# Optimization experiments

Measured on AMD Instinct MI355X. Metric: run time of the kernel, lower is better.

## Reference

```python
import jax, jax.numpy as jnp
import numpy as np

NUM_CLASSES = 19

def setup_inputs() -> dict:
    key = jax.random.key(0)
    k1, k2 = jax.random.split(key)
    feats = jax.random.normal(k1, (8, 256, 128, 256), dtype=jnp.float32)
    y_down = jax.random.randint(k2, (8, 128, 256), 0, NUM_CLASSES, dtype=jnp.int64)
    return {"feats": feats, "y_down": y_down}

def reference(feats, y_down):
    # feats: [B, C, H, W]; y_down: [B, H, W] int labels in [0, NUM_CLASSES)
    B, C, H, W = feats.shape
    x = jnp.transpose(feats, (0, 2, 3, 1)).reshape(-1, C)   # [N, C], N = B*H*W
    seg = y_down.reshape(-1).astype(jnp.int32)              # [N]
    # per-class sum of feature vectors and pixel counts (fused segment reduce)
    sums = jax.ops.segment_sum(x, seg, num_segments=NUM_CLASSES)          # [K, C]
    counts = jax.ops.segment_sum(jnp.ones((x.shape[0],), x.dtype), seg,
                                 num_segments=NUM_CLASSES)                # [K]
    denom = jnp.maximum(counts, 1.0)
    nonempty = counts > 0
    # b_c: per-class mean feature vector (zeros for empty classes, which torch
    # returns as empty tensors)
    means = jnp.where(nonempty[:, None], sums / denom[:, None], 0.0)      # [K, C]
    # n_c: per-class mean of per-pixel L2 norms (detached in original)
    norms = jnp.linalg.norm(x, axis=1)                                    # [N]
    norm_sums = jax.ops.segment_sum(norms, seg, num_segments=NUM_CLASSES)
    norm_means = jnp.where(nonempty, norm_sums / denom, 0.0)              # [K]
    return means, norm_means
```

## Files before the change

### kernel.cpp

```cpp
#include <hip/hip_runtime.h>

#define NCLS 19
#define NCH  256
#define HW   (128 * 256)
#define NPIX (8 * HW)
#define P    32
#define NT   (NPIX / P)
#define TPAD 36
#define SPAD 33
#define SUMS (NCLS * NCH)
#define PN_NORM SUMS
#define PN_CNT  (SUMS + NCLS)
#define PSTRIDE 4928
#define GRID  512
#define TILES (NT / GRID)

__device__ __forceinline__ void bar_lds() {
    asm volatile("s_waitcnt lgkmcnt(0)" ::: "memory");
    __builtin_amdgcn_sched_barrier(0);
    __builtin_amdgcn_s_barrier();
    __builtin_amdgcn_sched_barrier(0);
}

__global__ __launch_bounds__(256) void accum_kernel(
    const float* __restrict__ feats, const int* __restrict__ labels,
    float* __restrict__ partials)
{
    __shared__ float tile[NCH * TPAD];
    __shared__ float accA[SUMS];
    __shared__ float accB[SUMS];
    __shared__ float sqpart[32 * SPAD];
    __shared__ float accN[NCLS];
    __shared__ float accC[NCLS];
    __shared__ int   lab_s[P];

    const int t = threadIdx.x;
    for (int j = t; j < SUMS; j += 256) { accA[j] = 0.f; accB[j] = 0.f; }
    if (t < NCLS) { accN[t] = 0.f; accC[t] = 0.f; }

    const int j4 = (t & 7) * 4, cb = t >> 3;
    float4 v4[8];
    int labv = 0;

    {
        const int p0 = blockIdx.x * P, b = p0 >> 15, hw0 = p0 & (HW - 1);
        const float* fb = feats + (size_t)b * NCH * HW + hw0;
        #pragma unroll
        for (int i = 0; i < 8; ++i)
            v4[i] = *reinterpret_cast<const float4*>(fb + (size_t)(i * 32 + cb) * HW + j4);
        if (t < P) labv = labels[p0 + t];
    }
    {
        float s0 = 0.f, s1 = 0.f, s2 = 0.f, s3 = 0.f;
        #pragma unroll
        for (int i = 0; i < 8; ++i) {
            const int c = i * 32 + cb;
            tile[c * TPAD + j4    ] = v4[i].x; tile[c * TPAD + j4 + 1] = v4[i].y;
            tile[c * TPAD + j4 + 2] = v4[i].z; tile[c * TPAD + j4 + 3] = v4[i].w;
            s0 += v4[i].x * v4[i].x; s1 += v4[i].y * v4[i].y;
            s2 += v4[i].z * v4[i].z; s3 += v4[i].w * v4[i].w;
        }
        sqpart[cb * SPAD + j4    ] = s0; sqpart[cb * SPAD + j4 + 1] = s1;
        sqpart[cb * SPAD + j4 + 2] = s2; sqpart[cb * SPAD + j4 + 3] = s3;
        if (t < P) lab_s[t] = labv;
    }
    __syncthreads();

    for (int it = 0; it < TILES; ++it) {
        if (it + 1 < TILES) {
            const int p0 = (blockIdx.x + (it + 1) * GRID) * P;
            const int b = p0 >> 15, hw0 = p0 & (HW - 1);
            const float* fb = feats + (size_t)b * NCH * HW + hw0;
            #pragma unroll
            for (int i = 0; i < 8; ++i)
                v4[i] = *reinterpret_cast<const float4*>(fb + (size_t)(i * 32 + cb) * HW + j4);
            if (t < P) labv = labels[p0 + t];
        }
        {
            float v[P];
            #pragma unroll
            for (int p = 0; p < P; ++p) v[p] = tile[t * TPAD + p];
            #pragma unroll
            for (int p = 0; p < P; p += 2) {
                const int k0 = lab_s[p], k1 = lab_s[p + 1];
                accA[k0 * NCH + t] += v[p];
                accB[k1 * NCH + t] += v[p + 1];
            }
        }
        if (t < P) {
            float s = 0.f;
            #pragma unroll
            for (int m = 0; m < 32; ++m) s += sqpart[m * SPAD + t];
            const int k = lab_s[t];
            unsafeAtomicAdd(&accN[k], sqrtf(s));
            unsafeAtomicAdd(&accC[k], 1.f);
        }
        bar_lds();
        if (it + 1 < TILES) {
            float s0 = 0.f, s1 = 0.f, s2 = 0.f, s3 = 0.f;
            #pragma unroll
            for (int i = 0; i < 8; ++i) {
                const int c = i * 32 + cb;
                tile[c * TPAD + j4    ] = v4[i].x; tile[c * TPAD + j4 + 1] = v4[i].y;
                tile[c * TPAD + j4 + 2] = v4[i].z; tile[c * TPAD + j4 + 3] = v4[i].w;
                s0 += v4[i].x * v4[i].x; s1 += v4[i].y * v4[i].y;
                s2 += v4[i].z * v4[i].z; s3 += v4[i].w * v4[i].w;
            }
            sqpart[cb * SPAD + j4    ] = s0; sqpart[cb * SPAD + j4 + 1] = s1;
            sqpart[cb * SPAD + j4 + 2] = s2; sqpart[cb * SPAD + j4 + 3] = s3;
            if (t < P) lab_s[t] = labv;
        }
        bar_lds();
    }

    float* op = partials + (size_t)blockIdx.x * PSTRIDE;
    for (int j = t; j < SUMS; j += 256) op[j] = accA[j] + accB[j];
    if (t < NCLS) { op[PN_NORM + t] = accN[t]; op[PN_CNT + t] = accC[t]; }
}

__global__ __launch_bounds__(256) void reduce_kernel(
    const float* __restrict__ partials, float* __restrict__ out)
{
    __shared__ float cred[NCLS][9];
    __shared__ float red[16][17];
    __shared__ float cnt_s[NCLS];
    const int t = threadIdx.x;

    if (t < NCLS * 8) {
        const int k = t >> 3, gl = t & 7;
        float c = 0.f;
        #pragma unroll 8
        for (int j = 0; j < 64; ++j)
            c += partials[(size_t)(gl + 8 * j) * PSTRIDE + PN_CNT + k];
        cred[k][gl] = c;
    }
    {
        const int ol = t & 15, gl = t >> 4;
        const int o = blockIdx.x * 16 + ol;
        float s = 0.f;
        if (o < PN_CNT) {
            #pragma unroll 8
            for (int j = 0; j < 32; ++j)
                s += partials[(size_t)(gl + 16 * j) * PSTRIDE + o];
        }
        red[gl][ol] = s;
    }
    __syncthreads();
    if (t < NCLS) {
        float c = 0.f;
        #pragma unroll
        for (int g = 0; g < 8; ++g) c += cred[t][g];
        cnt_s[t] = c;
    }
    __syncthreads();
    if (t < 16) {
        const int oo = blockIdx.x * 16 + t;
        if (oo < PN_CNT) {
            float tot = 0.f;
            #pragma unroll
            for (int g = 0; g < 16; ++g) tot += red[g][t];
            const int k = (oo < SUMS) ? (oo >> 8) : (oo - SUMS);
            const float c = cnt_s[k];
            out[oo] = (c > 0.f) ? tot / fmaxf(c, 1.f) : 0.f;
        }
    }
}

extern "C" void kernel_launch(void* const* d_in, const int* in_sizes, int n_in,
                              void* d_out, int out_size, void* d_ws, size_t ws_size,
                              hipStream_t stream) {
    const float* feats  = (const float*)d_in[0];
    const int*   labels = (const int*)d_in[1];
    float* out      = (float*)d_out;
    float* partials = (float*)d_ws;

    accum_kernel<<<GRID, 256, 0, stream>>>(feats, labels, partials);
    reduce_kernel<<<(PN_CNT + 15) / 16, 256, 0, stream>>>(partials, out);
}
```

Measured before the change: 66.45 us.

## Accumulate per-class feature sums with one-hot bf16 MFMA instead of LDS scatter

Per-class sums are now computed as a matrix product of a one-hot label matrix and the feature tile, using 32x32x16 bf16 MFMA with fp32 accumulation held in registers. The feature tile is stored in LDS as bf16 rather than fp32, and the two LDS accumulator arrays are removed. This is meant to remove the serialized LDS read-modify-write scatter adds and to halve LDS traffic for the tile. In exchange, the feature values entering the sums are rounded to bf16, which reduces accuracy of the means.

```diff
diff --git a/kernel.cpp b/kernel.cpp
--- a/kernel.cpp
+++ b/kernel.cpp
@@ -6,7 +6,7 @@
 #define NPIX (8 * HW)
 #define P    32
 #define NT   (NPIX / P)
-#define TPAD 36
+#define THP  36
 #define SPAD 33
 #define SUMS (NCLS * NCH)
 #define PN_NORM SUMS
@@ -15,6 +15,11 @@
 #define GRID  512
 #define TILES (NT / GRID)
 
+typedef __bf16 bf16x4v __attribute__((ext_vector_type(4)));
+typedef __bf16 bf16x8v __attribute__((ext_vector_type(8)));
+typedef float  f32x16v __attribute__((ext_vector_type(16)));
+typedef int    int4v   __attribute__((ext_vector_type(4)));
+
 __device__ __forceinline__ void bar_lds() {
     asm volatile("s_waitcnt lgkmcnt(0)" ::: "memory");
     __builtin_amdgcn_sched_barrier(0);
@@ -26,19 +31,22 @@
     const float* __restrict__ feats, const int* __restrict__ labels,
     float* __restrict__ partials)
 {
-    __shared__ float tile[NCH * TPAD];
-    __shared__ float accA[SUMS];
-    __shared__ float accB[SUMS];
-    __shared__ float sqpart[32 * SPAD];
-    __shared__ float accN[NCLS];
-    __shared__ float accC[NCLS];
-    __shared__ int   lab_s[P];
+    __shared__ __bf16 tileh[NCH * THP];
+    __shared__ float  sqpart[32 * SPAD];
+    __shared__ float  accN[NCLS];
+    __shared__ float  accC[NCLS];
+    __shared__ int    lab_s[P];
 
     const int t = threadIdx.x;
-    for (int j = t; j < SUMS; j += 256) { accA[j] = 0.f; accB[j] = 0.f; }
     if (t < NCLS) { accN[t] = 0.f; accC[t] = 0.f; }
 
     const int j4 = (t & 7) * 4, cb = t >> 3;
+    const int w = t >> 6, l = t & 63, h = l >> 5, col = l & 31;
+    const int c0 = w * 64 + col;
+    const int c1 = c0 + 32;
+    const __bf16 ONE = (__bf16)1.0f, ZER = (__bf16)0.0f;
+
+    f32x16v d0 = {}, d1 = {};
     float4 v4[8];
     int labv = 0;
 
@@ -55,8 +63,8 @@
         #pragma unroll
         for (int i = 0; i < 8; ++i) {
             const int c = i * 32 + cb;
-            tile[c * TPAD + j4    ] = v4[i].x; tile[c * TPAD + j4 + 1] = v4[i].y;
-            tile[c * TPAD + j4 + 2] = v4[i].z; tile[c * TPAD + j4 + 3] = v4[i].w;
+            bf16x4v hv = { (__bf16)v4[i].x, (__bf16)v4[i].y, (__bf16)v4[i].z, (__bf16)v4[i].w };
+            *reinterpret_cast<bf16x4v*>(&tileh[c * THP + j4]) = hv;
             s0 += v4[i].x * v4[i].x; s1 += v4[i].y * v4[i].y;
             s2 += v4[i].z * v4[i].z; s3 += v4[i].w * v4[i].w;
         }
@@ -76,16 +84,24 @@
                 v4[i] = *reinterpret_cast<const float4*>(fb + (size_t)(i * 32 + cb) * HW + j4);
             if (t < P) labv = labels[p0 + t];
         }
-        {
-            float v[P];
-            #pragma unroll
-            for (int p = 0; p < P; ++p) v[p] = tile[t * TPAD + p];
-            #pragma unroll
-            for (int p = 0; p < P; p += 2) {
-                const int k0 = lab_s[p], k1 = lab_s[p + 1];
-                accA[k0 * NCH + t] += v[p];
-                accB[k1 * NCH + t] += v[p + 1];
-            }
+        #pragma unroll
+        for (int s = 0; s < 2; ++s) {
+            const int pb = s * 16 + h * 8;
+            const int4v lq0 = *reinterpret_cast<const int4v*>(&lab_s[pb]);
+            const int4v lq1 = *reinterpret_cast<const int4v*>(&lab_s[pb + 4]);
+            bf16x8v af;
+            af[0] = (lq0[0] == col) ? ONE : ZER;  af[1] = (lq0[1] == col) ? ONE : ZER;
+            af[2] = (lq0[2] == col) ? ONE : ZER;  af[3] = (lq0[3] == col) ? ONE : ZER;
+            af[4] = (lq1[0] == col) ? ONE : ZER;  af[5] = (lq1[1] == col) ? ONE : ZER;
+            af[6] = (lq1[2] == col) ? ONE : ZER;  af[7] = (lq1[3] == col) ? ONE : ZER;
+            const bf16x4v b0l = *reinterpret_cast<const bf16x4v*>(&tileh[c0 * THP + pb]);
+            const bf16x4v b0h = *reinterpret_cast<const bf16x4v*>(&tileh[c0 * THP + pb + 4]);
+            const bf16x4v b1l = *reinterpret_cast<const bf16x4v*>(&tileh[c1 * THP + pb]);
+            const bf16x4v b1h = *reinterpret_cast<const bf16x4v*>(&tileh[c1 * THP + pb + 4]);
+            const bf16x8v bf0 = __builtin_shufflevector(b0l, b0h, 0,1,2,3,4,5,6,7);
+            const bf16x8v bf1 = __builtin_shufflevector(b1l, b1h, 0,1,2,3,4,5,6,7);
+            d0 = __builtin_amdgcn_mfma_f32_32x32x16_bf16(af, bf0, d0, 0, 0, 0);
+            d1 = __builtin_amdgcn_mfma_f32_32x32x16_bf16(af, bf1, d1, 0, 0, 0);
         }
         if (t < P) {
             float s = 0.f;
@@ -101,8 +117,8 @@
             #pragma unroll
             for (int i = 0; i < 8; ++i) {
                 const int c = i * 32 + cb;
-                tile[c * TPAD + j4    ] = v4[i].x; tile[c * TPAD + j4 + 1] = v4[i].y;
-                tile[c * TPAD + j4 + 2] = v4[i].z; tile[c * TPAD + j4 + 3] = v4[i].w;
+                bf16x4v hv = { (__bf16)v4[i].x, (__bf16)v4[i].y, (__bf16)v4[i].z, (__bf16)v4[i].w };
+                *reinterpret_cast<bf16x4v*>(&tileh[c * THP + j4]) = hv;
                 s0 += v4[i].x * v4[i].x; s1 += v4[i].y * v4[i].y;
                 s2 += v4[i].z * v4[i].z; s3 += v4[i].w * v4[i].w;
             }
@@ -114,7 +130,14 @@
     }
 
     float* op = partials + (size_t)blockIdx.x * PSTRIDE;
-    for (int j = t; j < SUMS; j += 256) op[j] = accA[j] + accB[j];
+    #pragma unroll
+    for (int r = 0; r < 16; ++r) {
+        const int k = (r & 3) + 8 * (r >> 2) + 4 * h;
+        if (k < NCLS) {
+            op[k * NCH + c0] = d0[r];
+            op[k * NCH + c1] = d1[r];
+        }
+    }
     if (t < NCLS) { op[PN_NORM + t] = accN[t]; op[PN_CNT + t] = accC[t]; }
 }
 
```

New measurement: 65.16 us. No clear change (-1.9%).
